# Kernel optimization log

Hardware: AMD Instinct MI355X
Metric: run time of the kernel (lower is better)

## Reference

```python
import jax, jax.numpy as jnp
import numpy as np

OT_REG = 0.1
OT_ITERS = 10
LN_EPS = 1e-5


def layernorm(x, g, b):
    m = jnp.mean(x, axis=-1, keepdims=True)
    v = jnp.mean((x - m) ** 2, axis=-1, keepdims=True)
    return (x - m) * jax.lax.rsqrt(v + LN_EPS) * g + b


def sinkhorn(C, epsilon, iters):
    # standard Sinkhorn: kernel exp(C/eps), alternate row/col normalization
    Q = jnp.exp(C / epsilon)  # [Na,B,La,Lb]
    def body(_, Q):
        Q = Q / jnp.sum(Q, axis=-1, keepdims=True)
        Q = Q / jnp.sum(Q, axis=-2, keepdims=True)
        return Q
    return jax.lax.fori_loop(0, iters, body, Q)


def setup_inputs() -> dict:
    key = jax.random.key(0)
    ks = jax.random.split(key, 16)
    Na, La, B, Lb, Din, H = 32, 32, 64, 32, 768, 768
    s = 0.02
    return {
        "entity_cls": jax.random.normal(ks[0], (Na, Din), jnp.float32),
        "entity_tokens": jax.random.normal(ks[1], (Na, La, Din), jnp.float32),
        "mention_cls": jax.random.normal(ks[2], (B, Din), jnp.float32),
        "mention_tokens": jax.random.normal(ks[3], (B, Lb, Din), jnp.float32),
        "Wq": jax.random.normal(ks[4], (Din, H), jnp.float32) * s,
        "bq": jnp.zeros((H,), jnp.float32),
        "Wk": jax.random.normal(ks[5], (Din, H), jnp.float32) * s,
        "bk": jnp.zeros((H,), jnp.float32),
        "Wv": jax.random.normal(ks[6], (Din, H), jnp.float32) * s,
        "bv": jnp.zeros((H,), jnp.float32),
        "ln1_g": jnp.ones((H,), jnp.float32),
        "ln1_b": jnp.zeros((H,), jnp.float32),
        "Wcls": jax.random.normal(ks[7], (Din, H), jnp.float32) * s,
        "bcls": jnp.zeros((H,), jnp.float32),
        "Wsp": jax.random.normal(ks[8], (H, 1), jnp.float32) * s,
        "bsp": jnp.zeros((1,), jnp.float32),
        "ln2_g": jnp.ones((H,), jnp.float32),
        "ln2_b": jnp.zeros((H,), jnp.float32),
    }


def reference(entity_cls, entity_tokens, mention_cls, mention_tokens,
              Wq, bq, Wk, bk, Wv, bv, ln1_g, ln1_b,
              Wcls, bcls, Wsp, bsp, ln2_g, ln2_b):
    # projections
    q = entity_tokens @ Wq + bq      # [Na,La,H]
    k = mention_tokens @ Wk + bk     # [B,Lb,H]
    v = mention_tokens @ Wv + bv     # [B,Lb,H]

    # cross-batch cosine similarity: [Na,B,La,Lb]
    qn = q / jnp.maximum(jnp.linalg.norm(q, axis=-1, keepdims=True), 1e-8)
    kn = k / jnp.maximum(jnp.linalg.norm(k, axis=-1, keepdims=True), 1e-8)
    C = jnp.einsum('aid,bjd->abij', qn, kn)

    # Sinkhorn on detached cost (torch uses C.detach())
    T = sinkhorn(jax.lax.stop_gradient(C), OT_REG, OT_ITERS)
    # F.normalize(dim=-1): L2 normalize last dim
    T = T / jnp.maximum(jnp.linalg.norm(T, axis=-1, keepdims=True), 1e-12)

    # attention + residual + layernorm: [Na,B,La,H]
    attended = jnp.einsum('abij,bjd->abid', T, v) + q[:, None, :, :]
    attended = layernorm(attended, ln1_g, ln1_b)

    # softpool over token dim (-2)
    w = jax.nn.softmax(attended @ Wsp + bsp, axis=-2)   # [Na,B,La,1]
    pooled = jnp.sum(attended * w, axis=-2)             # [Na,B,H]
    context = layernorm(pooled, ln2_g, ln2_b)

    # matching scores
    ecls = entity_cls @ Wcls + bcls                     # [Na,H]
    g2l = jnp.sum(ecls[:, None, :] * context, axis=-1)  # [Na,B]
    g2l = g2l.T                                         # [B,Na]
    g2g = mention_cls @ entity_cls.T                    # [B,Na]
    return (g2l + g2g) * 0.5
```

## Files before the change

### kernel.cpp

```cpp
#include <hip/hip_runtime.h>
#include <math.h>


typedef __attribute__((ext_vector_type(8))) short bfrag8;
typedef __attribute__((ext_vector_type(4))) float f32x4;

__device__ __forceinline__ unsigned short f2bf(float x) {
  union { float f; unsigned u; } v; v.f = x;
  unsigned r = v.u + 0x7fffu + ((v.u >> 16) & 1u);
  return (unsigned short)(r >> 16);
}

__global__ __launch_bounds__(256) void prep_kernel(
    const float* __restrict__ a0, const float* __restrict__ a1, const float* __restrict__ a2,
    unsigned short* __restrict__ o0, unsigned short* __restrict__ o1, unsigned short* __restrict__ o2,
    float* __restrict__ nrm,
    const float* __restrict__ W0, const float* __restrict__ W1,
    const float* __restrict__ W2, const float* __restrict__ W3,
    unsigned short* __restrict__ T0, unsigned short* __restrict__ T1,
    unsigned short* __restrict__ T2, unsigned short* __restrict__ T3) {
  __shared__ float t[32][33];
  int bx = blockIdx.x;
  if (bx < 2331) {
    if (bx < 2328) {
      const float* in; unsigned short* out; int i, n4;
      if (bx < 768)       { in = a0; out = o0; i = bx * 256 + threadIdx.x;          n4 = 196608; }
      else if (bx < 2304) { in = a1; out = o1; i = (bx - 768) * 256 + threadIdx.x;  n4 = 393216; }
      else                { in = a2; out = o2; i = (bx - 2304) * 256 + threadIdx.x; n4 = 6144; }
      if (i >= n4) return;
      float4 f = ((const float4*)in)[i];
      ushort4 o;
      o.x = f2bf(f.x); o.y = f2bf(f.y); o.z = f2bf(f.z); o.w = f2bf(f.w);
      ((ushort4*)out)[i] = o;
    } else {
      int i = (bx - 2328) * 256 + threadIdx.x;
      if (i < 768) ((float4*)nrm)[i] = make_float4(0.f, 0.f, 0.f, 0.f);
    }
    return;
  }
  int idx = bx - 2331;
  int z = idx / 576, r2 = idx % 576;
  int tby = r2 / 24, tbx = r2 % 24;
  const float* W = (z == 0) ? W0 : (z == 1) ? W1 : (z == 2) ? W2 : W3;
  unsigned short* O = (z == 0) ? T0 : (z == 1) ? T1 : (z == 2) ? T2 : T3;
  const int gx = tbx * 32, gy = tby * 32;
  const int tx = threadIdx.x & 31, ty = threadIdx.x >> 5;
#pragma unroll
  for (int u = 0; u < 4; ++u) {
    int row = ty + u * 8;
    t[row][tx] = W[(size_t)(gy + row) * 768 + gx + tx];
  }
  __syncthreads();
#pragma unroll
  for (int u = 0; u < 4; ++u) {
    int row = ty + u * 8;
    O[(size_t)(gx + row) * 768 + gy + tx] = f2bf(t[tx][row]);
  }
}

__global__ __launch_bounds__(256) void proj_gemm_kernel(
    const unsigned short* __restrict__ Ae, const unsigned short* __restrict__ Am,
    const unsigned short* __restrict__ Acls,
    const unsigned short* __restrict__ WqT, const unsigned short* __restrict__ WkT,
    const unsigned short* __restrict__ WvT, const unsigned short* __restrict__ WclsT,
    const float* __restrict__ bq, const float* __restrict__ bk,
    const float* __restrict__ bv, const float* __restrict__ bcls,
    unsigned short* __restrict__ qb, unsigned short* __restrict__ qT,
    unsigned short* __restrict__ kb, unsigned short* __restrict__ vT,
    float* __restrict__ ecls, float* __restrict__ iq_sq, float* __restrict__ ik_sq) {
  const int z = blockIdx.z;
  const int M = (z == 0) ? 1024 : (z == 3) ? 32 : 2048;
  const int bm = blockIdx.y * 128;
  if (bm >= M) return;
  const unsigned short* A = (z == 3) ? Acls : (z == 0) ? Ae : Am;
  const unsigned short* B = (z == 0) ? WqT : (z == 1) ? WkT : (z == 2) ? WvT : WclsT;
  const float* bias = (z == 0) ? bq : (z == 1) ? bk : (z == 2) ? bv : bcls;

  __shared__ unsigned short As[128 * 64];
  __shared__ unsigned short Bs[128 * 64];
  const int t = threadIdx.x;
  const int bn = blockIdx.x * 128;
  const int l = t & 63, w = t >> 6;
  const int wm = w & 1, wn = w >> 1;

  f32x4 acc[4][4];
#pragma unroll
  for (int mi = 0; mi < 4; ++mi)
#pragma unroll
    for (int nj = 0; nj < 4; ++nj) { f32x4 zz = {0.f, 0.f, 0.f, 0.f}; acc[mi][nj] = zz; }

  for (int k0 = 0; k0 < 768; k0 += 64) {
    __syncthreads();
#pragma unroll
    for (int u = 0; u < 4; ++u) {
      int c = t + u * 256;
      int row = c >> 3, kc = c & 7;
      int gm = bm + row; gm = gm < M ? gm : M - 1;
      int4 av = *(const int4*)(A + (size_t)gm * 768 + k0 + kc * 8);
      *(int4*)(As + row * 64 + ((kc ^ (row & 7)) * 8)) = av;
      int4 bv4 = *(const int4*)(B + (size_t)(bn + row) * 768 + k0 + kc * 8);
      *(int4*)(Bs + row * 64 + ((kc ^ (row & 7)) * 8)) = bv4;
    }
    __syncthreads();
#pragma unroll
    for (int kk = 0; kk < 2; ++kk) {
      bfrag8 af[4], bf[4];
      const int kc = kk * 4 + (l >> 4);
#pragma unroll
      for (int mi = 0; mi < 4; ++mi) {
        int arow = wm * 64 + mi * 16 + (l & 15);
        af[mi] = *(const bfrag8*)(As + arow * 64 + ((kc ^ (arow & 7)) * 8));
      }
#pragma unroll
      for (int nj = 0; nj < 4; ++nj) {
        int brow = wn * 64 + nj * 16 + (l & 15);
        bf[nj] = *(const bfrag8*)(Bs + brow * 64 + ((kc ^ (brow & 7)) * 8));
      }
#pragma unroll
      for (int mi = 0; mi < 4; ++mi)
#pragma unroll
        for (int nj = 0; nj < 4; ++nj)
          acc[mi][nj] = __builtin_amdgcn_mfma_f32_16x16x32_bf16(af[mi], bf[nj], acc[mi][nj], 0, 0, 0);
    }
  }

  const int col = l & 15, rq = l >> 4;
  float p[4][4] = {};
#pragma unroll
  for (int mi = 0; mi < 4; ++mi) {
#pragma unroll
    for (int nj = 0; nj < 4; ++nj) {
      int gn = bn + wn * 64 + nj * 16 + col;
      float bs = bias[gn];
#pragma unroll
      for (int r = 0; r < 4; ++r) {
        int gm = bm + wm * 64 + mi * 16 + rq * 4 + r;
        if (gm >= M) continue;
        float val = acc[mi][nj][r] + bs;
        if (z < 2) p[mi][r] += val * val;
        unsigned short bfv = f2bf(val);
        if (z == 0) {
          qb[(size_t)gm * 768 + gn] = bfv;
          int at = gm >> 5, j = gm & 31;
          qT[((size_t)at * 768 + gn) * 32 + j] = bfv;
        } else if (z == 1) kb[(size_t)gm * 768 + gn] = bfv;
        else if (z == 2) {
          int bb = gm >> 5, j = gm & 31;
          vT[((size_t)bb * 768 + gn) * 32 + j] = bfv;
        } else ecls[(size_t)gm * 768 + gn] = val;
      }
    }
  }
  if (z < 2) {
    float* nrm = (z == 0) ? iq_sq : ik_sq;
#pragma unroll
    for (int mi = 0; mi < 4; ++mi)
#pragma unroll
      for (int r = 0; r < 4; ++r) {
        float s = p[mi][r];
        s += __shfl_xor(s, 1); s += __shfl_xor(s, 2);
        s += __shfl_xor(s, 4); s += __shfl_xor(s, 8);
        if (col == 0) {
          int gm = bm + wm * 64 + mi * 16 + rq * 4 + r;
          atomicAdd(&nrm[gm], s);
        }
      }
  }
}

__global__ __launch_bounds__(256) void cos_sink_kernel(
    const unsigned short* __restrict__ qb, const unsigned short* __restrict__ kb,
    const float* __restrict__ iq_sq, const float* __restrict__ ik_sq,
    unsigned short* __restrict__ Tg,
    const float* __restrict__ ln1_g, const float* __restrict__ ln1_b,
    const float* __restrict__ Wsp, const float* __restrict__ bsp,
    const float* __restrict__ ln2_g, const float* __restrict__ ln2_b,
    const float* __restrict__ ecls,
    const float* __restrict__ entity_cls, const float* __restrict__ mention_cls,
    float* __restrict__ gwv, float* __restrict__ auxgab,
    float4* __restrict__ cons, float* __restrict__ g2g) {
  __shared__ unsigned short As[128 * 64];
  __shared__ unsigned short Bs[64 * 64];
  __shared__ float ldsIq[128], ldsIk[64];
  const int t = threadIdx.x;

  if (blockIdx.y == 8) {
    float* redf = (float*)As;
    const int a2 = blockIdx.x;
    float sgw = 0.f, sbw = 0.f, sga = 0.f, sba = 0.f;
#pragma unroll
    for (int cc = 0; cc < 3; ++cc) {
      int h = t + cc * 256;
      float g1 = ln1_g[h], b1 = ln1_b[h], wsp = Wsp[h];
      float ec = ecls[(size_t)a2 * 768 + h];
      float gw = g1 * wsp;
      float gab = ln2_g[h] * ec;
      if (a2 == 0) gwv[h] = gw;
      auxgab[(size_t)a2 * 768 + h] = gab;
      sgw += gw; sbw += b1 * wsp; sga += gab; sba += ln2_b[h] * ec;
    }
#pragma unroll
    for (int m = 1; m < 64; m <<= 1) {
      sgw += __shfl_xor(sgw, m); sbw += __shfl_xor(sbw, m);
      sga += __shfl_xor(sga, m); sba += __shfl_xor(sba, m);
    }
    const int wv = t >> 6, ln = t & 63;
    if (ln == 0) { redf[wv * 4] = sgw; redf[wv * 4 + 1] = sbw; redf[wv * 4 + 2] = sga; redf[wv * 4 + 3] = sba; }
    __syncthreads();
    if (t == 0) {
      float4 c;
      c.x = redf[0] + redf[4] + redf[8] + redf[12];
      c.y = redf[1] + redf[5] + redf[9] + redf[13] + bsp[0];
      c.z = redf[2] + redf[6] + redf[10] + redf[14];
      c.w = redf[3] + redf[7] + redf[11] + redf[15];
      cons[a2] = c;
    }
    const float* ea = entity_cls + (size_t)a2 * 768;
    for (int bb = wv; bb < 64; bb += 4) {
      const float* mbp = mention_cls + (size_t)bb * 768;
      float s = 0.f;
#pragma unroll
      for (int u = 0; u < 12; ++u) s += mbp[ln * 12 + u] * ea[ln * 12 + u];
#pragma unroll
      for (int m = 1; m < 64; m <<= 1) s += __shfl_xor(s, m);
      if (ln == 0) g2g[bb * 32 + a2] = s;
    }
    return;
  }

  const int bn = blockIdx.x * 64, bm = blockIdx.y * 128;
  const int l = t & 63, w = t >> 6;
  const int wm = w & 1, wn = w >> 1;
  const int cg = l & 15, rq = l >> 4;

  if (t < 128) ldsIq[t] = iq_sq[bm + t];
  else if (t < 192) ldsIk[t - 128] = ik_sq[bn + t - 128];

  f32x4 acc[4][2];
#pragma unroll
  for (int mi = 0; mi < 4; ++mi)
#pragma unroll
    for (int nj = 0; nj < 2; ++nj) { f32x4 zz = {0.f, 0.f, 0.f, 0.f}; acc[mi][nj] = zz; }

  for (int k0 = 0; k0 < 768; k0 += 64) {
    __syncthreads();
#pragma unroll
    for (int u = 0; u < 4; ++u) {
      int c = t + u * 256;
      int row = c >> 3, kc = c & 7;
      int4 av = *(const int4*)(qb + (size_t)(bm + row) * 768 + k0 + kc * 8);
      *(int4*)(As + row * 64 + ((kc ^ (row & 7)) * 8)) = av;
    }
#pragma unroll
    for (int u = 0; u < 2; ++u) {
      int c = t + u * 256;
      int row = c >> 3, kc = c & 7;
      int4 bv4 = *(const int4*)(kb + (size_t)(bn + row) * 768 + k0 + kc * 8);
      *(int4*)(Bs + row * 64 + ((kc ^ (row & 7)) * 8)) = bv4;
    }
    __syncthreads();
#pragma unroll
    for (int kk = 0; kk < 2; ++kk) {
      bfrag8 af[4], bf[2];
      const int kc = kk * 4 + rq;
#pragma unroll
      for (int mi = 0; mi < 4; ++mi) {
        int arow = wm * 64 + mi * 16 + cg;
        af[mi] = *(const bfrag8*)(As + arow * 64 + ((kc ^ (arow & 7)) * 8));
      }
#pragma unroll
      for (int nj = 0; nj < 2; ++nj) {
        int brow = wn * 32 + nj * 16 + cg;
        bf[nj] = *(const bfrag8*)(Bs + brow * 64 + ((kc ^ (brow & 7)) * 8));
      }
#pragma unroll
      for (int mi = 0; mi < 4; ++mi)
#pragma unroll
        for (int nj = 0; nj < 2; ++nj)
          acc[mi][nj] = __builtin_amdgcn_mfma_f32_16x16x32_bf16(af[mi], bf[nj], acc[mi][nj], 0, 0, 0);
    }
  }

  float irow[4][4], icol[2];
#pragma unroll
  for (int mi = 0; mi < 4; ++mi)
#pragma unroll
    for (int r = 0; r < 4; ++r) {
      float s = ldsIq[wm * 64 + mi * 16 + rq * 4 + r];
      irow[mi][r] = 1.0f / fmaxf(sqrtf(s), 1e-8f);
    }
#pragma unroll
  for (int nj = 0; nj < 2; ++nj) {
    float s = ldsIk[wn * 32 + nj * 16 + cg];
    icol[nj] = 1.0f / fmaxf(sqrtf(s), 1e-8f);
  }
#pragma unroll
  for (int mi = 0; mi < 4; ++mi)
#pragma unroll
    for (int nj = 0; nj < 2; ++nj)
#pragma unroll
      for (int r = 0; r < 4; ++r)
        acc[mi][nj][r] = __expf(acc[mi][nj][r] * irow[mi][r] * icol[nj] * 10.0f);

  for (int it = 0; it < 10; ++it) {
#pragma unroll
    for (int mi = 0; mi < 4; ++mi)
#pragma unroll
      for (int r = 0; r < 4; ++r) {
        float rs = acc[mi][0][r] + acc[mi][1][r];
        rs += __shfl_xor(rs, 1); rs += __shfl_xor(rs, 2);
        rs += __shfl_xor(rs, 4); rs += __shfl_xor(rs, 8);
        float rinv = __builtin_amdgcn_rcpf(rs);
        acc[mi][0][r] *= rinv; acc[mi][1][r] *= rinv;
      }
#pragma unroll
    for (int ta = 0; ta < 2; ++ta)
#pragma unroll
      for (int nj = 0; nj < 2; ++nj) {
        float cs = acc[2 * ta][nj][0] + acc[2 * ta][nj][1] + acc[2 * ta][nj][2] + acc[2 * ta][nj][3]
                 + acc[2 * ta + 1][nj][0] + acc[2 * ta + 1][nj][1] + acc[2 * ta + 1][nj][2] + acc[2 * ta + 1][nj][3];
        cs += __shfl_xor(cs, 16); cs += __shfl_xor(cs, 32);
        float cinv = __builtin_amdgcn_rcpf(cs);
#pragma unroll
        for (int mi2 = 0; mi2 < 2; ++mi2)
#pragma unroll
          for (int r = 0; r < 4; ++r) acc[2 * ta + mi2][nj][r] *= cinv;
      }
  }

#pragma unroll
  for (int mi = 0; mi < 4; ++mi)
#pragma unroll
    for (int r = 0; r < 4; ++r) {
      float ss = acc[mi][0][r] * acc[mi][0][r] + acc[mi][1][r] * acc[mi][1][r];
      ss += __shfl_xor(ss, 1); ss += __shfl_xor(ss, 2);
      ss += __shfl_xor(ss, 4); ss += __shfl_xor(ss, 8);
      float tinv = 1.0f / fmaxf(sqrtf(ss), 1e-12f);
      acc[mi][0][r] *= tinv; acc[mi][1][r] *= tinv;
    }

  const int b_idx = (bn >> 5) + wn;
#pragma unroll
  for (int mi = 0; mi < 4; ++mi) {
    const int a_idx = (bm >> 5) + wm * 2 + (mi >> 1);
    unsigned short* base = Tg + (((size_t)b_idx * 32 + a_idx) << 10);
    const int ri0 = (mi & 1) * 16 + rq * 4;
#pragma unroll
    for (int nj = 0; nj < 2; ++nj)
#pragma unroll
      for (int r = 0; r < 4; ++r)
        base[(ri0 + r) * 32 + nj * 16 + cg] = f2bf(acc[mi][nj][r]);
  }
}

__global__ __launch_bounds__(256) void attn_kernel(
    const unsigned short* __restrict__ Tg,
    const unsigned short* __restrict__ vT,
    const unsigned short* __restrict__ qT,
    const float* __restrict__ gwv,
    const float* __restrict__ ln1_g, const float* __restrict__ ln1_b,
    const float* __restrict__ auxgab,
    const float4* __restrict__ cons,
    const float* __restrict__ g2g,
    float* __restrict__ out) {
  __shared__ unsigned short vLds[768 * 32];
  const int t = threadIdx.x;
  const int w = t >> 6, l = t & 63;
  const int b = blockIdx.x >> 3;
  const int a = ((blockIdx.x & 7) << 2) + w;
  const int pair = b * 32 + a;
  const int cg = l & 15, rq = l >> 4;

  {
    const int4* src = (const int4*)(vT + (size_t)b * 768 * 32);
    int4* dst = (int4*)vLds;
#pragma unroll
    for (int u = 0; u < 12; ++u) dst[t + u * 256] = src[t + u * 256];
  }
  __syncthreads();

  const unsigned short* Tp = Tg + ((size_t)pair << 10);
  bfrag8 af[2], afI[2];
#pragma unroll
  for (int mi = 0; mi < 2; ++mi) {
    int row = mi * 16 + cg;
    af[mi] = *(const bfrag8*)(Tp + row * 32 + rq * 8);
    bfrag8 fI;
#pragma unroll
    for (int u = 0; u < 8; ++u) fI[u] = (row == rq * 8 + u) ? (short)0x3F80 : (short)0;
    afI[mi] = fI;
  }

  const unsigned short* qTa = qT + (size_t)a * 768 * 32;
  const float4 cc4 = cons[a];

  float s1[2][4] = {}, s2[2][4] = {}, a1[2][4] = {};
#pragma unroll 4
  for (int nj = 0; nj < 48; ++nj) {
    int h = nj * 16 + cg;
    bfrag8 vf = *(const bfrag8*)(vLds + h * 32 + rq * 8);
    bfrag8 qf = *(const bfrag8*)(qTa + (size_t)h * 32 + rq * 8);
    float gw = gwv[h];
#pragma unroll
    for (int mi = 0; mi < 2; ++mi) {
      f32x4 zz = {0.f, 0.f, 0.f, 0.f};
      f32x4 p = __builtin_amdgcn_mfma_f32_16x16x32_bf16(af[mi], vf, zz, 0, 0, 0);
      f32x4 x4 = __builtin_amdgcn_mfma_f32_16x16x32_bf16(afI[mi], qf, p, 0, 0, 0);
#pragma unroll
      for (int r = 0; r < 4; ++r) {
        float x = x4[r];
        s1[mi][r] += x; s2[mi][r] += x * x; a1[mi][r] += x * gw;
      }
    }
  }
#pragma unroll
  for (int m = 1; m < 16; m <<= 1) {
#pragma unroll
    for (int mi = 0; mi < 2; ++mi)
#pragma unroll
      for (int r = 0; r < 4; ++r) {
        s1[mi][r] += __shfl_xor(s1[mi][r], m);
        s2[mi][r] += __shfl_xor(s2[mi][r], m);
        a1[mi][r] += __shfl_xor(a1[mi][r], m);
      }
  }

  float uu[2][4], c0 = 0.f;
  {
    float mean[2][4], rstd[2][4], logit[2][4];
#pragma unroll
    for (int mi = 0; mi < 2; ++mi)
#pragma unroll
      for (int r = 0; r < 4; ++r) {
        float m1 = s1[mi][r] * (1.0f / 768.0f);
        float var = s2[mi][r] * (1.0f / 768.0f) - m1 * m1;
        float rs = rsqrtf(var + 1e-5f);
        mean[mi][r] = m1; rstd[mi][r] = rs;
        logit[mi][r] = rs * (a1[mi][r] - m1 * cc4.x) + cc4.y;
      }
    float mx = logit[0][0];
#pragma unroll
    for (int mi = 0; mi < 2; ++mi)
#pragma unroll
      for (int r = 0; r < 4; ++r) mx = fmaxf(mx, logit[mi][r]);
    mx = fmaxf(mx, __shfl_xor(mx, 16)); mx = fmaxf(mx, __shfl_xor(mx, 32));
    float se = 0.f, ee[2][4];
#pragma unroll
    for (int mi = 0; mi < 2; ++mi)
#pragma unroll
      for (int r = 0; r < 4; ++r) { ee[mi][r] = __expf(logit[mi][r] - mx); se += ee[mi][r]; }
    se += __shfl_xor(se, 16); se += __shfl_xor(se, 32);
    const float sinv = __builtin_amdgcn_rcpf(se);
#pragma unroll
    for (int mi = 0; mi < 2; ++mi)
#pragma unroll
      for (int r = 0; r < 4; ++r) {
        uu[mi][r] = ee[mi][r] * sinv * rstd[mi][r];
        c0 += uu[mi][r] * mean[mi][r];
      }
    c0 += __shfl_xor(c0, 16); c0 += __shfl_xor(c0, 32);
  }

  const float* gabp = auxgab + (size_t)a * 768;
  float ps = 0.f, pq = 0.f, spc = 0.f;
#pragma unroll 4
  for (int nj = 0; nj < 48; ++nj) {
    int h = nj * 16 + cg;
    bfrag8 vf = *(const bfrag8*)(vLds + h * 32 + rq * 8);
    bfrag8 qf = *(const bfrag8*)(qTa + (size_t)h * 32 + rq * 8);
    float pp = 0.f;
#pragma unroll
    for (int mi = 0; mi < 2; ++mi) {
      f32x4 zz = {0.f, 0.f, 0.f, 0.f};
      f32x4 p = __builtin_amdgcn_mfma_f32_16x16x32_bf16(af[mi], vf, zz, 0, 0, 0);
      f32x4 x4 = __builtin_amdgcn_mfma_f32_16x16x32_bf16(afI[mi], qf, p, 0, 0, 0);
#pragma unroll
      for (int r = 0; r < 4; ++r) pp += uu[mi][r] * x4[r];
    }
    pp += __shfl_xor(pp, 16); pp += __shfl_xor(pp, 32);
    float pooled = ln1_g[h] * (pp - c0) + ln1_b[h];
    ps += pooled; pq += pooled * pooled; spc += pooled * gabp[h];
  }
#pragma unroll
  for (int m = 1; m < 16; m <<= 1) {
    ps += __shfl_xor(ps, m); pq += __shfl_xor(pq, m); spc += __shfl_xor(spc, m);
  }
  const float m2 = ps * (1.0f / 768.0f);
  const float var2 = pq * (1.0f / 768.0f) - m2 * m2;
  const float rs2 = rsqrtf(var2 + 1e-5f);
  float tot = rs2 * (spc - m2 * cc4.z) + cc4.w + g2g[b * 32 + a];
  if (l == 0) out[b * 32 + a] = 0.5f * tot;
}

extern "C" void kernel_launch(void* const* d_in, const int* in_sizes, int n_in,
                              void* d_out, int out_size, void* d_ws, size_t ws_size,
                              hipStream_t stream) {
  const float* entity_cls     = (const float*)d_in[0];
  const float* entity_tokens  = (const float*)d_in[1];
  const float* mention_cls    = (const float*)d_in[2];
  const float* mention_tokens = (const float*)d_in[3];
  const float* Wq = (const float*)d_in[4];   const float* bq = (const float*)d_in[5];
  const float* Wk = (const float*)d_in[6];   const float* bk = (const float*)d_in[7];
  const float* Wv = (const float*)d_in[8];   const float* bv = (const float*)d_in[9];
  const float* ln1_g = (const float*)d_in[10]; const float* ln1_b = (const float*)d_in[11];
  const float* Wcls = (const float*)d_in[12];  const float* bcls = (const float*)d_in[13];
  const float* Wsp = (const float*)d_in[14];   const float* bsp = (const float*)d_in[15];
  const float* ln2_g = (const float*)d_in[16]; const float* ln2_b = (const float*)d_in[17];
  float* out = (float*)d_out;

  float* ws     = (float*)d_ws;
  float* ecls   = ws;
  float* iq_sq  = ecls + 24576;
  float* ik_sq  = iq_sq + 1024;
  float* gwv    = ik_sq + 2048;
  float* auxgab = gwv + 768;
  float* g2g    = auxgab + 24576;
  float4* cons  = (float4*)(g2g + 2048);
  unsigned short* qb = (unsigned short*)(cons + 32);
  unsigned short* qT = qb + 786432;
  unsigned short* kb = qT + 786432;
  unsigned short* vT = kb + 1572864;
  char* R = (char*)(vT + 1572864);
  unsigned short* Ae    = (unsigned short*)R;
  unsigned short* Am    = Ae + 786432;
  unsigned short* Acls  = Am + 1572864;
  unsigned short* WqT   = Acls + 24576;
  unsigned short* WkT   = WqT + 589824;
  unsigned short* WvT   = WkT + 589824;
  unsigned short* WclsT = WvT + 589824;
  unsigned short* Tg = (unsigned short*)R;

  dim3 blk(256);
  prep_kernel<<<dim3(4635), blk, 0, stream>>>(
      entity_tokens, mention_tokens, entity_cls, Ae, Am, Acls, iq_sq,
      Wq, Wk, Wv, Wcls, WqT, WkT, WvT, WclsT);
  proj_gemm_kernel<<<dim3(6, 16, 4), blk, 0, stream>>>(
      Ae, Am, Acls, WqT, WkT, WvT, WclsT, bq, bk, bv, bcls,
      qb, qT, kb, vT, ecls, iq_sq, ik_sq);
  cos_sink_kernel<<<dim3(32, 9), blk, 0, stream>>>(
      qb, kb, iq_sq, ik_sq, Tg,
      ln1_g, ln1_b, Wsp, bsp, ln2_g, ln2_b, ecls, entity_cls, mention_cls,
      gwv, auxgab, cons, g2g);
  attn_kernel<<<dim3(512), blk, 0, stream>>>(
      Tg, vT, qT, gwv, ln1_g, ln1_b, auxgab, cons, g2g, out);
}
```

Before: 185.8 us.

## Fuse all stages into one persistent cooperative kernel with grid syncs

Replaces the four separate kernel launches (prep, projection GEMM, cosine+Sinkhorn, attention/pool) with a single cooperative mega-kernel of 256 blocks that loops over each stage's tasks and separates stages with grid-wide syncs. This is meant to remove inter-kernel launch gaps and tail effects. In exchange, the fixed grid forces multiple task passes per stage, adds grid barrier cost, and the union shared memory plus the larger combined kernel may reduce occupancy. The old multi-launch path is kept as a fallback if the cooperative launch fails.

```diff
diff --git a/kernel.cpp b/kernel.cpp
--- a/kernel.cpp
+++ b/kernel.cpp
@@ -1,5 +1,8 @@
 #include <hip/hip_runtime.h>
+#include <hip/hip_cooperative_groups.h>
 #include <math.h>
+
+namespace cg = cooperative_groups;
 
 
 typedef __attribute__((ext_vector_type(8))) short bfrag8;
@@ -10,6 +13,7 @@
   unsigned r = v.u + 0x7fffu + ((v.u >> 16) & 1u);
   return (unsigned short)(r >> 16);
 }
+
 
 __global__ __launch_bounds__(256) void prep_kernel(
     const float* __restrict__ a0, const float* __restrict__ a1, const float* __restrict__ a2,
@@ -354,15 +358,11 @@
 }
 
 __global__ __launch_bounds__(256) void attn_kernel(
-    const unsigned short* __restrict__ Tg,
-    const unsigned short* __restrict__ vT,
-    const unsigned short* __restrict__ qT,
-    const float* __restrict__ gwv,
+    const unsigned short* __restrict__ Tg, const unsigned short* __restrict__ vT,
+    const unsigned short* __restrict__ qT, const float* __restrict__ gwv,
     const float* __restrict__ ln1_g, const float* __restrict__ ln1_b,
-    const float* __restrict__ auxgab,
-    const float4* __restrict__ cons,
-    const float* __restrict__ g2g,
-    float* __restrict__ out) {
+    const float* __restrict__ auxgab, const float4* __restrict__ cons,
+    const float* __restrict__ g2g, float* __restrict__ out) {
   __shared__ unsigned short vLds[768 * 32];
   const int t = threadIdx.x;
   const int w = t >> 6, l = t & 63;
@@ -490,6 +490,471 @@
   const float rs2 = rsqrtf(var2 + 1e-5f);
   float tot = rs2 * (spc - m2 * cc4.z) + cc4.w + g2g[b * 32 + a];
   if (l == 0) out[b * 32 + a] = 0.5f * tot;
+}
+
+
+struct MegaParams {
+  const float *entity_cls, *entity_tokens, *mention_cls, *mention_tokens;
+  const float *Wq, *bq, *Wk, *bk, *Wv, *bv;
+  const float *ln1_g, *ln1_b, *Wcls, *bcls, *Wsp, *bsp, *ln2_g, *ln2_b;
+  float *ecls, *iq_sq, *ik_sq, *gwv, *auxgab, *g2g;
+  float4 *cons;
+  unsigned short *qb, *qT, *kb, *vT;
+  unsigned short *Ae, *Am, *Acls, *WqT, *WkT, *WvT, *WclsT, *Tg;
+  float *out;
+};
+
+union SharedU {
+  struct { float t[32][33]; } prep;
+  struct { unsigned short As[128 * 64]; unsigned short Bs[128 * 64]; } proj;
+  struct { unsigned short As[128 * 64]; unsigned short Bs[64 * 64];
+           float iq[128]; float ik[64]; } cs;
+  struct { unsigned short v[768 * 32]; } attn;
+};
+
+__global__ __launch_bounds__(256) void mega_kernel(MegaParams p) {
+  __shared__ SharedU sh;
+  cg::grid_group grid = cg::this_grid();
+  const int t = threadIdx.x;
+  const int nb = gridDim.x;
+
+  for (int task = blockIdx.x; task < 4635; task += nb) {
+    if (task < 2328) {
+      const float* in; unsigned short* out; int i, n4;
+      if (task < 768)       { in = p.entity_tokens;  out = p.Ae;   i = task * 256 + t;          n4 = 196608; }
+      else if (task < 2304) { in = p.mention_tokens; out = p.Am;   i = (task - 768) * 256 + t;  n4 = 393216; }
+      else                  { in = p.entity_cls;     out = p.Acls; i = (task - 2304) * 256 + t; n4 = 6144; }
+      if (i < n4) {
+        float4 f = ((const float4*)in)[i];
+        ushort4 o;
+        o.x = f2bf(f.x); o.y = f2bf(f.y); o.z = f2bf(f.z); o.w = f2bf(f.w);
+        ((ushort4*)out)[i] = o;
+      }
+    } else if (task < 2331) {
+      int i = (task - 2328) * 256 + t;
+      if (i < 768) ((float4*)p.iq_sq)[i] = make_float4(0.f, 0.f, 0.f, 0.f);
+    } else {
+      int idx = task - 2331;
+      int z = idx / 576, r2 = idx % 576;
+      int tby = r2 / 24, tbx = r2 % 24;
+      const float* W = (z == 0) ? p.Wq : (z == 1) ? p.Wk : (z == 2) ? p.Wv : p.Wcls;
+      unsigned short* O = (z == 0) ? p.WqT : (z == 1) ? p.WkT : (z == 2) ? p.WvT : p.WclsT;
+      const int gx = tbx * 32, gy = tby * 32;
+      const int tx = t & 31, ty = t >> 5;
+      __syncthreads();
+#pragma unroll
+      for (int u = 0; u < 4; ++u) {
+        int row = ty + u * 8;
+        sh.prep.t[row][tx] = W[(size_t)(gy + row) * 768 + gx + tx];
+      }
+      __syncthreads();
+#pragma unroll
+      for (int u = 0; u < 4; ++u) {
+        int row = ty + u * 8;
+        O[(size_t)(gx + row) * 768 + gy + tx] = f2bf(sh.prep.t[tx][row]);
+      }
+    }
+  }
+  grid.sync();
+
+  for (int vb = blockIdx.x; vb < 384; vb += nb) {
+    const int bxp = vb % 6, byp = (vb / 6) % 16, z = vb / 96;
+    const int M = (z == 0) ? 1024 : (z == 3) ? 32 : 2048;
+    const int bm = byp * 128;
+    if (bm >= M) continue;
+    const unsigned short* A = (z == 3) ? p.Acls : (z == 0) ? p.Ae : p.Am;
+    const unsigned short* B = (z == 0) ? p.WqT : (z == 1) ? p.WkT : (z == 2) ? p.WvT : p.WclsT;
+    const float* bias = (z == 0) ? p.bq : (z == 1) ? p.bk : (z == 2) ? p.bv : p.bcls;
+    const int bn = bxp * 128;
+    const int l = t & 63, w = t >> 6;
+    const int wm = w & 1, wn = w >> 1;
+
+    f32x4 acc[4][4];
+#pragma unroll
+    for (int mi = 0; mi < 4; ++mi)
+#pragma unroll
+      for (int nj = 0; nj < 4; ++nj) { f32x4 zz = {0.f, 0.f, 0.f, 0.f}; acc[mi][nj] = zz; }
+
+    for (int k0 = 0; k0 < 768; k0 += 64) {
+      __syncthreads();
+#pragma unroll
+      for (int u = 0; u < 4; ++u) {
+        int c = t + u * 256;
+        int row = c >> 3, kc = c & 7;
+        int gm = bm + row; gm = gm < M ? gm : M - 1;
+        int4 av = *(const int4*)(A + (size_t)gm * 768 + k0 + kc * 8);
+        *(int4*)(sh.proj.As + row * 64 + ((kc ^ (row & 7)) * 8)) = av;
+        int4 bv4 = *(const int4*)(B + (size_t)(bn + row) * 768 + k0 + kc * 8);
+        *(int4*)(sh.proj.Bs + row * 64 + ((kc ^ (row & 7)) * 8)) = bv4;
+      }
+      __syncthreads();
+#pragma unroll
+      for (int kk = 0; kk < 2; ++kk) {
+        bfrag8 af[4], bf[4];
+        const int kc = kk * 4 + (l >> 4);
+#pragma unroll
+        for (int mi = 0; mi < 4; ++mi) {
+          int arow = wm * 64 + mi * 16 + (l & 15);
+          af[mi] = *(const bfrag8*)(sh.proj.As + arow * 64 + ((kc ^ (arow & 7)) * 8));
+        }
+#pragma unroll
+        for (int nj = 0; nj < 4; ++nj) {
+          int brow = wn * 64 + nj * 16 + (l & 15);
+          bf[nj] = *(const bfrag8*)(sh.proj.Bs + brow * 64 + ((kc ^ (brow & 7)) * 8));
+        }
+#pragma unroll
+        for (int mi = 0; mi < 4; ++mi)
+#pragma unroll
+          for (int nj = 0; nj < 4; ++nj)
+            acc[mi][nj] = __builtin_amdgcn_mfma_f32_16x16x32_bf16(af[mi], bf[nj], acc[mi][nj], 0, 0, 0);
+      }
+    }
+
+    const int col = l & 15, rq = l >> 4;
+    float pr[4][4] = {};
+#pragma unroll
+    for (int mi = 0; mi < 4; ++mi) {
+#pragma unroll
+      for (int nj = 0; nj < 4; ++nj) {
+        int gn = bn + wn * 64 + nj * 16 + col;
+        float bs = bias[gn];
+#pragma unroll
+        for (int r = 0; r < 4; ++r) {
+          int gm = bm + wm * 64 + mi * 16 + rq * 4 + r;
+          if (gm >= M) continue;
+          float val = acc[mi][nj][r] + bs;
+          if (z < 2) pr[mi][r] += val * val;
+          unsigned short bfv = f2bf(val);
+          if (z == 0) {
+            p.qb[(size_t)gm * 768 + gn] = bfv;
+            int at = gm >> 5, j = gm & 31;
+            p.qT[((size_t)at * 768 + gn) * 32 + j] = bfv;
+          } else if (z == 1) p.kb[(size_t)gm * 768 + gn] = bfv;
+          else if (z == 2) {
+            int bb = gm >> 5, j = gm & 31;
+            p.vT[((size_t)bb * 768 + gn) * 32 + j] = bfv;
+          } else p.ecls[(size_t)gm * 768 + gn] = val;
+        }
+      }
+    }
+    if (z < 2) {
+      float* nrm = (z == 0) ? p.iq_sq : p.ik_sq;
+#pragma unroll
+      for (int mi = 0; mi < 4; ++mi)
+#pragma unroll
+        for (int r = 0; r < 4; ++r) {
+          float s = pr[mi][r];
+          s += __shfl_xor(s, 1); s += __shfl_xor(s, 2);
+          s += __shfl_xor(s, 4); s += __shfl_xor(s, 8);
+          if (col == 0) {
+            int gm = bm + wm * 64 + mi * 16 + rq * 4 + r;
+            atomicAdd(&nrm[gm], s);
+          }
+        }
+    }
+  }
+  grid.sync();
+
+  for (int vb = blockIdx.x; vb < 288; vb += nb) {
+    if (vb < 256) {
+      const int bn = (vb & 31) * 64, bm = (vb >> 5) * 128;
+      const int l = t & 63, w = t >> 6;
+      const int wm = w & 1, wn = w >> 1;
+      const int cg2 = l & 15, rq = l >> 4;
+
+      __syncthreads();
+      if (t < 128) sh.cs.iq[t] = p.iq_sq[bm + t];
+      else if (t < 192) sh.cs.ik[t - 128] = p.ik_sq[bn + t - 128];
+
+      f32x4 acc[4][2];
+#pragma unroll
+      for (int mi = 0; mi < 4; ++mi)
+#pragma unroll
+        for (int nj = 0; nj < 2; ++nj) { f32x4 zz = {0.f, 0.f, 0.f, 0.f}; acc[mi][nj] = zz; }
+
+      for (int k0 = 0; k0 < 768; k0 += 64) {
+        __syncthreads();
+#pragma unroll
+        for (int u = 0; u < 4; ++u) {
+          int c = t + u * 256;
+          int row = c >> 3, kc = c & 7;
+          int4 av = *(const int4*)(p.qb + (size_t)(bm + row) * 768 + k0 + kc * 8);
+          *(int4*)(sh.cs.As + row * 64 + ((kc ^ (row & 7)) * 8)) = av;
+        }
+#pragma unroll
+        for (int u = 0; u < 2; ++u) {
+          int c = t + u * 256;
+          int row = c >> 3, kc = c & 7;
+          int4 bv4 = *(const int4*)(p.kb + (size_t)(bn + row) * 768 + k0 + kc * 8);
+          *(int4*)(sh.cs.Bs + row * 64 + ((kc ^ (row & 7)) * 8)) = bv4;
+        }
+        __syncthreads();
+#pragma unroll
+        for (int kk = 0; kk < 2; ++kk) {
+          bfrag8 af[4], bf[2];
+          const int kc = kk * 4 + rq;
+#pragma unroll
+          for (int mi = 0; mi < 4; ++mi) {
+            int arow = wm * 64 + mi * 16 + cg2;
+            af[mi] = *(const bfrag8*)(sh.cs.As + arow * 64 + ((kc ^ (arow & 7)) * 8));
+          }
+#pragma unroll
+          for (int nj = 0; nj < 2; ++nj) {
+            int brow = wn * 32 + nj * 16 + cg2;
+            bf[nj] = *(const bfrag8*)(sh.cs.Bs + brow * 64 + ((kc ^ (brow & 7)) * 8));
+          }
+#pragma unroll
+          for (int mi = 0; mi < 4; ++mi)
+#pragma unroll
+            for (int nj = 0; nj < 2; ++nj)
+              acc[mi][nj] = __builtin_amdgcn_mfma_f32_16x16x32_bf16(af[mi], bf[nj], acc[mi][nj], 0, 0, 0);
+        }
+      }
+
+      float irow[4][4], icol[2];
+#pragma unroll
+      for (int mi = 0; mi < 4; ++mi)
+#pragma unroll
+        for (int r = 0; r < 4; ++r) {
+          float s = sh.cs.iq[wm * 64 + mi * 16 + rq * 4 + r];
+          irow[mi][r] = 1.0f / fmaxf(sqrtf(s), 1e-8f);
+        }
+#pragma unroll
+      for (int nj = 0; nj < 2; ++nj) {
+        float s = sh.cs.ik[wn * 32 + nj * 16 + cg2];
+        icol[nj] = 1.0f / fmaxf(sqrtf(s), 1e-8f);
+      }
+#pragma unroll
+      for (int mi = 0; mi < 4; ++mi)
+#pragma unroll
+        for (int nj = 0; nj < 2; ++nj)
+#pragma unroll
+          for (int r = 0; r < 4; ++r)
+            acc[mi][nj][r] = __expf(acc[mi][nj][r] * irow[mi][r] * icol[nj] * 10.0f);
+
+      for (int it = 0; it < 10; ++it) {
+#pragma unroll
+        for (int mi = 0; mi < 4; ++mi)
+#pragma unroll
+          for (int r = 0; r < 4; ++r) {
+            float rs = acc[mi][0][r] + acc[mi][1][r];
+            rs += __shfl_xor(rs, 1); rs += __shfl_xor(rs, 2);
+            rs += __shfl_xor(rs, 4); rs += __shfl_xor(rs, 8);
+            float rinv = __builtin_amdgcn_rcpf(rs);
+            acc[mi][0][r] *= rinv; acc[mi][1][r] *= rinv;
+          }
+#pragma unroll
+        for (int ta = 0; ta < 2; ++ta)
+#pragma unroll
+          for (int nj = 0; nj < 2; ++nj) {
+            float cs = acc[2 * ta][nj][0] + acc[2 * ta][nj][1] + acc[2 * ta][nj][2] + acc[2 * ta][nj][3]
+                     + acc[2 * ta + 1][nj][0] + acc[2 * ta + 1][nj][1] + acc[2 * ta + 1][nj][2] + acc[2 * ta + 1][nj][3];
+            cs += __shfl_xor(cs, 16); cs += __shfl_xor(cs, 32);
+            float cinv = __builtin_amdgcn_rcpf(cs);
+#pragma unroll
+            for (int mi2 = 0; mi2 < 2; ++mi2)
+#pragma unroll
+              for (int r = 0; r < 4; ++r) acc[2 * ta + mi2][nj][r] *= cinv;
+          }
+      }
+
+#pragma unroll
+      for (int mi = 0; mi < 4; ++mi)
+#pragma unroll
+        for (int r = 0; r < 4; ++r) {
+          float ss = acc[mi][0][r] * acc[mi][0][r] + acc[mi][1][r] * acc[mi][1][r];
+          ss += __shfl_xor(ss, 1); ss += __shfl_xor(ss, 2);
+          ss += __shfl_xor(ss, 4); ss += __shfl_xor(ss, 8);
+          float tinv = 1.0f / fmaxf(sqrtf(ss), 1e-12f);
+          acc[mi][0][r] *= tinv; acc[mi][1][r] *= tinv;
+        }
+
+      const int b_idx = (bn >> 5) + wn;
+#pragma unroll
+      for (int mi = 0; mi < 4; ++mi) {
+        const int a_idx = (bm >> 5) + wm * 2 + (mi >> 1);
+        unsigned short* base = p.Tg + (((size_t)b_idx * 32 + a_idx) << 10);
+        const int ri0 = (mi & 1) * 16 + rq * 4;
+#pragma unroll
+        for (int nj = 0; nj < 2; ++nj)
+#pragma unroll
+          for (int r = 0; r < 4; ++r)
+            base[(ri0 + r) * 32 + nj * 16 + cg2] = f2bf(acc[mi][nj][r]);
+      }
+    } else {
+      float* redf = (float*)sh.cs.As;
+      const int a2 = vb - 256;
+      float sgw = 0.f, sbw = 0.f, sga = 0.f, sba = 0.f;
+#pragma unroll
+      for (int cc = 0; cc < 3; ++cc) {
+        int h = t + cc * 256;
+        float g1 = p.ln1_g[h], b1 = p.ln1_b[h], wsp = p.Wsp[h];
+        float ec = p.ecls[(size_t)a2 * 768 + h];
+        float gw = g1 * wsp;
+        float gab = p.ln2_g[h] * ec;
+        if (a2 == 0) p.gwv[h] = gw;
+        p.auxgab[(size_t)a2 * 768 + h] = gab;
+        sgw += gw; sbw += b1 * wsp; sga += gab; sba += p.ln2_b[h] * ec;
+      }
+#pragma unroll
+      for (int m = 1; m < 64; m <<= 1) {
+        sgw += __shfl_xor(sgw, m); sbw += __shfl_xor(sbw, m);
+        sga += __shfl_xor(sga, m); sba += __shfl_xor(sba, m);
+      }
+      const int wv = t >> 6, ln = t & 63;
+      __syncthreads();
+      if (ln == 0) { redf[wv * 4] = sgw; redf[wv * 4 + 1] = sbw; redf[wv * 4 + 2] = sga; redf[wv * 4 + 3] = sba; }
+      __syncthreads();
+      if (t == 0) {
+        float4 c;
+        c.x = redf[0] + redf[4] + redf[8] + redf[12];
+        c.y = redf[1] + redf[5] + redf[9] + redf[13] + p.bsp[0];
+        c.z = redf[2] + redf[6] + redf[10] + redf[14];
+        c.w = redf[3] + redf[7] + redf[11] + redf[15];
+        p.cons[a2] = c;
+      }
+      const float* ea = p.entity_cls + (size_t)a2 * 768;
+      for (int bb = wv; bb < 64; bb += 4) {
+        const float* mbp = p.mention_cls + (size_t)bb * 768;
+        float s = 0.f;
+#pragma unroll
+        for (int u = 0; u < 12; ++u) s += mbp[ln * 12 + u] * ea[ln * 12 + u];
+#pragma unroll
+        for (int m = 1; m < 64; m <<= 1) s += __shfl_xor(s, m);
+        if (ln == 0) p.g2g[bb * 32 + a2] = s;
+      }
+    }
+  }
+  grid.sync();
+
+  for (int vd = blockIdx.x; vd < 512; vd += nb) {
+    const int w = t >> 6, l = t & 63;
+    const int b = vd >> 3;
+    const int a = ((vd & 7) << 2) + w;
+    const int pair = b * 32 + a;
+    const int cg2 = l & 15, rq = l >> 4;
+
+    __syncthreads();
+    {
+      const int4* src = (const int4*)(p.vT + (size_t)b * 768 * 32);
+      int4* dst = (int4*)sh.attn.v;
+#pragma unroll
+      for (int u = 0; u < 12; ++u) dst[t + u * 256] = src[t + u * 256];
+    }
+    __syncthreads();
+
+    const unsigned short* Tp = p.Tg + ((size_t)pair << 10);
+    bfrag8 af[2], afI[2];
+#pragma unroll
+    for (int mi = 0; mi < 2; ++mi) {
+      int row = mi * 16 + cg2;
+      af[mi] = *(const bfrag8*)(Tp + row * 32 + rq * 8);
+      bfrag8 fI;
+#pragma unroll
+      for (int u = 0; u < 8; ++u) fI[u] = (row == rq * 8 + u) ? (short)0x3F80 : (short)0;
+      afI[mi] = fI;
+    }
+
+    const unsigned short* qTa = p.qT + (size_t)a * 768 * 32;
+    const float4 cc4 = p.cons[a];
+
+    float s1[2][4] = {}, s2[2][4] = {}, a1[2][4] = {};
+#pragma unroll 4
+    for (int nj = 0; nj < 48; ++nj) {
+      int h = nj * 16 + cg2;
+      bfrag8 vf = *(const bfrag8*)(sh.attn.v + h * 32 + rq * 8);
+      bfrag8 qf = *(const bfrag8*)(qTa + (size_t)h * 32 + rq * 8);
+      float gw = p.gwv[h];
+#pragma unroll
+      for (int mi = 0; mi < 2; ++mi) {
+        f32x4 zz = {0.f, 0.f, 0.f, 0.f};
+        f32x4 pp = __builtin_amdgcn_mfma_f32_16x16x32_bf16(af[mi], vf, zz, 0, 0, 0);
+        f32x4 x4 = __builtin_amdgcn_mfma_f32_16x16x32_bf16(afI[mi], qf, pp, 0, 0, 0);
+#pragma unroll
+        for (int r = 0; r < 4; ++r) {
+          float x = x4[r];
+          s1[mi][r] += x; s2[mi][r] += x * x; a1[mi][r] += x * gw;
+        }
+      }
+    }
+#pragma unroll
+    for (int m = 1; m < 16; m <<= 1) {
+#pragma unroll
+      for (int mi = 0; mi < 2; ++mi)
+#pragma unroll
+        for (int r = 0; r < 4; ++r) {
+          s1[mi][r] += __shfl_xor(s1[mi][r], m);
+          s2[mi][r] += __shfl_xor(s2[mi][r], m);
+          a1[mi][r] += __shfl_xor(a1[mi][r], m);
+        }
+    }
+
+    float uu[2][4], c0 = 0.f;
+    {
+      float mean[2][4], rstd[2][4], logit[2][4];
+#pragma unroll
+      for (int mi = 0; mi < 2; ++mi)
+#pragma unroll
+        for (int r = 0; r < 4; ++r) {
+          float m1 = s1[mi][r] * (1.0f / 768.0f);
+          float var = s2[mi][r] * (1.0f / 768.0f) - m1 * m1;
+          float rs = rsqrtf(var + 1e-5f);
+          mean[mi][r] = m1; rstd[mi][r] = rs;
+          logit[mi][r] = rs * (a1[mi][r] - m1 * cc4.x) + cc4.y;
+        }
+      float mx = logit[0][0];
+#pragma unroll
+      for (int mi = 0; mi < 2; ++mi)
+#pragma unroll
+        for (int r = 0; r < 4; ++r) mx = fmaxf(mx, logit[mi][r]);
+      mx = fmaxf(mx, __shfl_xor(mx, 16)); mx = fmaxf(mx, __shfl_xor(mx, 32));
+      float se = 0.f, ee[2][4];
+#pragma unroll
+      for (int mi = 0; mi < 2; ++mi)
+#pragma unroll
+        for (int r = 0; r < 4; ++r) { ee[mi][r] = __expf(logit[mi][r] - mx); se += ee[mi][r]; }
+      se += __shfl_xor(se, 16); se += __shfl_xor(se, 32);
+      const float sinv = __builtin_amdgcn_rcpf(se);
+#pragma unroll
+      for (int mi = 0; mi < 2; ++mi)
+#pragma unroll
+        for (int r = 0; r < 4; ++r) {
+          uu[mi][r] = ee[mi][r] * sinv * rstd[mi][r];
+          c0 += uu[mi][r] * mean[mi][r];
+        }
+      c0 += __shfl_xor(c0, 16); c0 += __shfl_xor(c0, 32);
+    }
+
+    const float* gabp = p.auxgab + (size_t)a * 768;
+    float ps = 0.f, pq = 0.f, spc = 0.f;
+#pragma unroll 4
+    for (int nj = 0; nj < 48; ++nj) {
+      int h = nj * 16 + cg2;
+      bfrag8 vf = *(const bfrag8*)(sh.attn.v + h * 32 + rq * 8);
+      bfrag8 qf = *(const bfrag8*)(qTa + (size_t)h * 32 + rq * 8);
+      float pp = 0.f;
+#pragma unroll
+      for (int mi = 0; mi < 2; ++mi) {
+        f32x4 zz = {0.f, 0.f, 0.f, 0.f};
+        f32x4 p2 = __builtin_amdgcn_mfma_f32_16x16x32_bf16(af[mi], vf, zz, 0, 0, 0);
+        f32x4 x4 = __builtin_amdgcn_mfma_f32_16x16x32_bf16(afI[mi], qf, p2, 0, 0, 0);
+#pragma unroll
+        for (int r = 0; r < 4; ++r) pp += uu[mi][r] * x4[r];
+      }
+      pp += __shfl_xor(pp, 16); pp += __shfl_xor(pp, 32);
+      float pooled = p.ln1_g[h] * (pp - c0) + p.ln1_b[h];
+      ps += pooled; pq += pooled * pooled; spc += pooled * gabp[h];
+    }
+#pragma unroll
+    for (int m = 1; m < 16; m <<= 1) {
+      ps += __shfl_xor(ps, m); pq += __shfl_xor(pq, m); spc += __shfl_xor(spc, m);
+    }
+    const float m2 = ps * (1.0f / 768.0f);
+    const float var2 = pq * (1.0f / 768.0f) - m2 * m2;
+    const float rs2 = rsqrtf(var2 + 1e-5f);
+    float tot = rs2 * (spc - m2 * cc4.z) + cc4.w + p.g2g[b * 32 + a];
+    if (l == 0) p.out[b * 32 + a] = 0.5f * tot;
+  }
 }
 
 extern "C" void kernel_launch(void* const* d_in, const int* in_sizes, int n_in,
@@ -530,17 +995,42 @@
   unsigned short* WclsT = WvT + 589824;
   unsigned short* Tg = (unsigned short*)R;
 
-  dim3 blk(256);
-  prep_kernel<<<dim3(4635), blk, 0, stream>>>(
-      entity_tokens, mention_tokens, entity_cls, Ae, Am, Acls, iq_sq,
-      Wq, Wk, Wv, Wcls, WqT, WkT, WvT, WclsT);
-  proj_gemm_kernel<<<dim3(6, 16, 4), blk, 0, stream>>>(
-      Ae, Am, Acls, WqT, WkT, WvT, WclsT, bq, bk, bv, bcls,
-      qb, qT, kb, vT, ecls, iq_sq, ik_sq);
-  cos_sink_kernel<<<dim3(32, 9), blk, 0, stream>>>(
-      qb, kb, iq_sq, ik_sq, Tg,
-      ln1_g, ln1_b, Wsp, bsp, ln2_g, ln2_b, ecls, entity_cls, mention_cls,
-      gwv, auxgab, cons, g2g);
-  attn_kernel<<<dim3(512), blk, 0, stream>>>(
-      Tg, vT, qT, gwv, ln1_g, ln1_b, auxgab, cons, g2g, out);
+  MegaParams p;
+  p.entity_cls = entity_cls; p.entity_tokens = entity_tokens;
+  p.mention_cls = mention_cls; p.mention_tokens = mention_tokens;
+  p.Wq = Wq; p.bq = bq; p.Wk = Wk; p.bk = bk; p.Wv = Wv; p.bv = bv;
+  p.ln1_g = ln1_g; p.ln1_b = ln1_b; p.Wcls = Wcls; p.bcls = bcls;
+  p.Wsp = Wsp; p.bsp = bsp; p.ln2_g = ln2_g; p.ln2_b = ln2_b;
+  p.ecls = ecls; p.iq_sq = iq_sq; p.ik_sq = ik_sq;
+  p.gwv = gwv; p.auxgab = auxgab; p.g2g = g2g; p.cons = cons;
+  p.qb = qb; p.qT = qT; p.kb = kb; p.vT = vT;
+  p.Ae = Ae; p.Am = Am; p.Acls = Acls;
+  p.WqT = WqT; p.WkT = WkT; p.WvT = WvT; p.WclsT = WclsT;
+  p.Tg = Tg;
+  p.out = out;
+
+  int maxPerCU = 0;
+  hipError_t qe = hipOccupancyMaxActiveBlocksPerMultiprocessor(
+      &maxPerCU, (const void*)mega_kernel, 256, 0);
+  hipError_t err = hipErrorUnknown;
+  if (qe == hipSuccess && maxPerCU >= 1) {
+    void* args[] = { &p };
+    err = hipLaunchCooperativeKernel((const void*)mega_kernel, dim3(256), dim3(256),
+                                     args, 0, stream);
+  }
+  if (err != hipSuccess) {
+    dim3 blk(256);
+    prep_kernel<<<dim3(4635), blk, 0, stream>>>(
+        entity_tokens, mention_tokens, entity_cls, Ae, Am, Acls, iq_sq,
+        Wq, Wk, Wv, Wcls, WqT, WkT, WvT, WclsT);
+    proj_gemm_kernel<<<dim3(6, 16, 4), blk, 0, stream>>>(
+        Ae, Am, Acls, WqT, WkT, WvT, WclsT, bq, bk, bv, bcls,
+        qb, qT, kb, vT, ecls, iq_sq, ik_sq);
+    cos_sink_kernel<<<dim3(32, 9), blk, 0, stream>>>(
+        qb, kb, iq_sq, ik_sq, Tg,
+        ln1_g, ln1_b, Wsp, bsp, ln2_g, ln2_b, ecls, entity_cls, mention_cls,
+        gwv, auxgab, cons, g2g);
+    attn_kernel<<<dim3(512), blk, 0, stream>>>(
+        Tg, vT, qT, gwv, ln1_g, ln1_b, auxgab, cons, g2g, out);
+  }
 }
```

Measured after the change: 354.7 us. 90.9% more time.
